# Kernel tuning notes

Measured on AMD Instinct MI355X. Metric: run time of the kernel, lower is better.

## Reference

```python
import jax, jax.numpy as jnp
import numpy as np

B, S, H = 2, 2048, 2048
NQ, NKV, DH = 16, 8, 128
EPS = 1e-6
ROPE_BASE = 10000.0


def setup_inputs() -> dict:
    key = jax.random.key(0)
    ks = jax.random.split(key, 6)
    hidden_states = jax.random.normal(ks[0], (B, S, H), dtype=jnp.float32)
    # real RoPE tables
    inv_freq = 1.0 / (ROPE_BASE ** (jnp.arange(0, DH, 2, dtype=jnp.float32) / DH))
    pos = jnp.arange(S, dtype=jnp.float32)
    freqs = pos[:, None] * inv_freq[None, :]              # [S, DH/2]
    emb = jnp.concatenate([freqs, freqs], axis=-1)        # [S, DH]
    cos = jnp.broadcast_to(jnp.cos(emb)[None], (B, S, DH))
    sin = jnp.broadcast_to(jnp.sin(emb)[None], (B, S, DH))
    # additive causal mask [1,1,S,S]
    causal = jnp.tril(jnp.ones((S, S), dtype=bool))
    attention_mask = jnp.where(causal, 0.0, jnp.finfo(jnp.float32).min)[None, None]
    q_w = jax.random.normal(ks[1], (H, H), dtype=jnp.float32) * 0.02
    k_w = jax.random.normal(ks[2], (NKV * DH, H), dtype=jnp.float32) * 0.02
    v_w = jax.random.normal(ks[3], (NKV * DH, H), dtype=jnp.float32) * 0.02
    o_w = jax.random.normal(ks[4], (H, H), dtype=jnp.float32) * 0.02
    return {"hidden_states": hidden_states, "cos": cos, "sin": sin,
            "attention_mask": attention_mask,
            "q_w": q_w, "k_w": k_w, "v_w": v_w, "o_w": o_w}


def _rotate_half(x):
    x1, x2 = jnp.split(x, 2, axis=-1)
    return jnp.concatenate([-x2, x1], axis=-1)


def _l2norm(x, eps=EPS):
    # weightless RMS norm over head_dim (Llama4TextL2Norm)
    return x * jax.lax.rsqrt(jnp.mean(x * x, axis=-1, keepdims=True) + eps)


def reference(hidden_states, cos, sin, attention_mask, q_w, k_w, v_w, o_w):
    b, s, _ = hidden_states.shape
    # projections (no bias) -> [B, n_heads, S, DH]
    q = jnp.einsum('bsh,dh->bsd', hidden_states, q_w).reshape(b, s, NQ, DH).transpose(0, 2, 1, 3)
    k = jnp.einsum('bsh,dh->bsd', hidden_states, k_w).reshape(b, s, NKV, DH).transpose(0, 2, 1, 3)
    v = jnp.einsum('bsh,dh->bsd', hidden_states, v_w).reshape(b, s, NKV, DH).transpose(0, 2, 1, 3)
    # NanoChat negates sin before standard HF rotary
    sin_e = (-sin)[:, None, :, :]   # [B,1,S,DH]
    cos_e = cos[:, None, :, :]
    q = q * cos_e + _rotate_half(q) * sin_e
    k = k * cos_e + _rotate_half(k) * sin_e
    # weightless QK RMS norm
    q = _l2norm(q)
    k = _l2norm(k)
    # GQA: repeat kv heads
    groups = NQ // NKV
    k = jnp.repeat(k, groups, axis=1)
    v = jnp.repeat(v, groups, axis=1)
    scaling = DH ** -0.5
    scores = jnp.einsum('bhqd,bhkd->bhqk', q, k) * scaling + attention_mask
    probs = jax.nn.softmax(scores, axis=-1)
    attn = jnp.einsum('bhqk,bhkd->bhqd', probs, v)           # [B,H,S,DH]
    attn = attn.transpose(0, 2, 1, 3).reshape(b, s, NQ * DH)
    out = jnp.einsum('bsd,hd->bsh', attn, o_w)
    return out
```

## Files before the change

kernel.cpp:

```cpp
#include <hip/hip_runtime.h>

typedef unsigned short ushort_t;
typedef __bf16 bf16x8 __attribute__((ext_vector_type(8)));
typedef float f32x4 __attribute__((ext_vector_type(4)));
typedef unsigned int u32x4 __attribute__((ext_vector_type(4)));
typedef unsigned short us4 __attribute__((ext_vector_type(4)));
typedef unsigned short us8 __attribute__((ext_vector_type(8)));

#define DEVINL __device__ __forceinline__

DEVINL ushort_t f2bf(float f) {
    unsigned u = __float_as_uint(f);
    u += 0x7FFF + ((u >> 16) & 1);
    return (ushort_t)(u >> 16);
}
DEVINL float bf2f(ushort_t h) { return __uint_as_float(((unsigned)h) << 16); }

DEVINL void gload_lds16(const void* g, void* l) {
    __builtin_amdgcn_global_load_lds(
        (const __attribute__((address_space(1))) void*)g,
        (__attribute__((address_space(3))) void*)l, 16, 0, 0);
}

DEVINL bf16x8 ld_frag(const ushort_t* p) {
    us8 v = *(const us8*)p;
    return __builtin_bit_cast(bf16x8, v);
}

#define BAR()     asm volatile("s_barrier" ::: "memory")
#define LGKM0()   asm volatile("s_waitcnt lgkmcnt(0)" ::: "memory")
#define VMCNT(n)  asm volatile("s_waitcnt vmcnt(" #n ")" ::: "memory")

#define BARRIER_KEEP4()  asm volatile("s_waitcnt vmcnt(4)\n\ts_barrier" ::: "memory")
#define BARRIER_KEEP8()  asm volatile("s_waitcnt vmcnt(8)\n\ts_barrier" ::: "memory")
#define BARRIER_KEEP0()  asm volatile("s_waitcnt vmcnt(0)\n\ts_barrier" ::: "memory")

__global__ __launch_bounds__(256) void convert_all(const f32x4* __restrict__ h,
                                                   const f32x4* __restrict__ qw,
                                                   const f32x4* __restrict__ kw,
                                                   const f32x4* __restrict__ vw,
                                                   const f32x4* __restrict__ ow,
                                                   us4* __restrict__ hb,
                                                   us4* __restrict__ wqkv,
                                                   us4* __restrict__ owb) {
    const int N0 = 2097152;
    const int N1 = 1048576;
    const int N2 = 524288;
    const int N3 = 524288;
    int i = blockIdx.x * 256 + threadIdx.x;
    const f32x4* src; us4* dst;
    if (i < N0)                               { src = h  + i;                 dst = hb + i; }
    else if ((i -= N0) < N1)                  { src = qw + i;                 dst = wqkv + i; }
    else if ((i -= N1) < N2)                  { src = kw + i;                 dst = wqkv + 1048576 + i; }
    else if ((i -= N2) < N3)                  { src = vw + i;                 dst = wqkv + 1572864 + i; }
    else                                      { i -= N3; src = ow + i;       dst = owb + i; }
    f32x4 f = *src;
    us4 o;
    o[0] = f2bf(f[0]); o[1] = f2bf(f[1]); o[2] = f2bf(f[2]); o[3] = f2bf(f[3]);
    *dst = o;
}

template <typename OutT>
__global__ __launch_bounds__(512, 2) void gemm256(const ushort_t* __restrict__ A,
                                                  const ushort_t* __restrict__ W,
                                                  OutT* __restrict__ C,
                                                  int N, int K) {
    __shared__ ushort_t As[2][256 * 64];
    __shared__ ushort_t Bs[2][256 * 64];
    const int t = threadIdx.x;
    const int lane = t & 63;
    const int quad = lane >> 4, l16 = lane & 15;
    const int wm = t >> 8, wn = (t >> 6) & 3;

    int bid = blockIdx.x;
    int xcd = bid & 7, j = bid >> 3;
    int tm, tn;
    if (N == 4096) { tm = (xcd >> 1) * 4 + (j >> 3); tn = (xcd & 1) * 8 + (j & 7); }
    else           { tm = xcd * 2 + (j >> 3);        tn = j & 7; }
    const int bm = tm * 256, bn = tn * 256;

    const int srow0 = t >> 3;
    const int sg0 = ((t & 7) ^ (srow0 & 7)) * 8;
    const int srow1 = srow0 + 64;
    const int sg1 = ((t & 7) ^ (srow1 & 7)) * 8;

    auto stageA = [&](int buf, int half, int k0) {
        gload_lds16(A + (size_t)(bm + half * 128 + srow0) * K + k0 + sg0,
                    &As[buf][half * 8192 + t * 8]);
        gload_lds16(A + (size_t)(bm + half * 128 + srow1) * K + k0 + sg1,
                    &As[buf][half * 8192 + 4096 + t * 8]);
    };
    auto stageB = [&](int buf, int half, int k0) {
        gload_lds16(W + (size_t)(bn + half * 128 + srow0) * K + k0 + sg0,
                    &Bs[buf][half * 8192 + t * 8]);
        gload_lds16(W + (size_t)(bn + half * 128 + srow1) * K + k0 + sg1,
                    &Bs[buf][half * 8192 + 4096 + t * 8]);
    };

    const int xsw = l16 & 7;
    const int arow = (wm * 128 + l16) * 64;
    const int brow = (wn * 64 + l16) * 64;
    const int ac0 = ((0 + quad) ^ xsw) * 8;
    const int ac1 = ((4 + quad) ^ xsw) * 8;

    auto ldA = [&](int buf, int mf, int kk) {
        return ld_frag(&As[buf][arow + mf * 1024 + (kk ? ac1 : ac0)]);
    };
    auto ldB = [&](int buf, int nf, int kk) {
        return ld_frag(&Bs[buf][brow + nf * 1024 + (kk ? ac1 : ac0)]);
    };

    f32x4 acc[8][4];
#pragma unroll
    for (int i = 0; i < 8; i++)
#pragma unroll
        for (int jj = 0; jj < 4; jj++) acc[i][jj] = f32x4{0.f, 0.f, 0.f, 0.f};

    const int NIT = K >> 6;
    stageA(0, 0, 0); stageA(0, 1, 0); stageB(0, 0, 0); stageB(0, 1, 0);
    VMCNT(4);
    stageB(1, 0, 64); stageB(1, 1, 64); stageA(1, 0, 64);
    VMCNT(6);
    BAR();

    bf16x8 a[4][2], b[4][2];
    for (int tt = 0; tt < NIT; ++tt) {
        const int buf = tt & 1;
        const int k2 = (tt + 2) << 6;

#pragma unroll
        for (int mt = 0; mt < 4; mt++) { a[mt][0] = ldA(buf, mt, 0); a[mt][1] = ldA(buf, mt, 1); }
#pragma unroll
        for (int nt = 0; nt < 4; nt++) { b[nt][0] = ldB(buf, nt, 0); b[nt][1] = ldB(buf, nt, 1); }
        if (tt + 1 < NIT) stageA(buf ^ 1, 1, (tt + 1) << 6);
        BAR(); LGKM0();
        __builtin_amdgcn_s_setprio(1);
#pragma unroll
        for (int mt = 0; mt < 4; mt++)
#pragma unroll
            for (int nt = 0; nt < 2; nt++)
#pragma unroll
                for (int kk = 0; kk < 2; kk++)
                    acc[mt][nt] = __builtin_amdgcn_mfma_f32_16x16x32_bf16(a[mt][kk], b[nt][kk], acc[mt][nt], 0, 0, 0);
        __builtin_amdgcn_s_setprio(0);
        LGKM0();
        BAR();

        if (tt + 2 < NIT) stageB(buf, 0, k2);
        BAR();
        __builtin_amdgcn_s_setprio(1);
#pragma unroll
        for (int mt = 0; mt < 4; mt++)
#pragma unroll
            for (int nt = 0; nt < 2; nt++)
#pragma unroll
                for (int kk = 0; kk < 2; kk++)
                    acc[mt][2 + nt] = __builtin_amdgcn_mfma_f32_16x16x32_bf16(a[mt][kk], b[2 + nt][kk], acc[mt][2 + nt], 0, 0, 0);
        __builtin_amdgcn_s_setprio(0);
        BAR();

#pragma unroll
        for (int mt = 0; mt < 4; mt++) { a[mt][0] = ldA(buf, 4 + mt, 0); a[mt][1] = ldA(buf, 4 + mt, 1); }
        if (tt + 2 < NIT) stageB(buf, 1, k2);
        BAR(); LGKM0();
        __builtin_amdgcn_s_setprio(1);
#pragma unroll
        for (int mt = 0; mt < 4; mt++)
#pragma unroll
            for (int nt = 0; nt < 2; nt++)
#pragma unroll
                for (int kk = 0; kk < 2; kk++)
                    acc[4 + mt][nt] = __builtin_amdgcn_mfma_f32_16x16x32_bf16(a[mt][kk], b[nt][kk], acc[4 + mt][nt], 0, 0, 0);
        __builtin_amdgcn_s_setprio(0);
        BAR();

        if (tt + 2 < NIT)      { stageA(buf, 0, k2); VMCNT(6); }
        else if (tt + 1 < NIT) { VMCNT(0); }
        BAR();
        __builtin_amdgcn_s_setprio(1);
#pragma unroll
        for (int mt = 0; mt < 4; mt++)
#pragma unroll
            for (int nt = 0; nt < 2; nt++)
#pragma unroll
                for (int kk = 0; kk < 2; kk++)
                    acc[4 + mt][2 + nt] = __builtin_amdgcn_mfma_f32_16x16x32_bf16(a[mt][kk], b[2 + nt][kk], acc[4 + mt][2 + nt], 0, 0, 0);
        __builtin_amdgcn_s_setprio(0);
        BAR();
    }

#pragma unroll
    for (int mf = 0; mf < 8; mf++)
#pragma unroll
        for (int nf = 0; nf < 4; nf++) {
            const int row = bm + wm * 128 + mf * 16 + quad * 4;
            const int col = bn + wn * 64 + nf * 16 + l16;
#pragma unroll
            for (int rr = 0; rr < 4; rr++) {
                float v = acc[mf][nf][rr];
                if constexpr (sizeof(OutT) == 2)
                    C[(size_t)(row + rr) * N + col] = (OutT)f2bf(v);
                else
                    C[(size_t)(row + rr) * N + col] = v;
            }
        }
}

__global__ __launch_bounds__(256) void rope_norm(const ushort_t* __restrict__ qkv,
                                                 const float* __restrict__ cosb,
                                                 const float* __restrict__ sinb,
                                                 ushort_t* __restrict__ q,
                                                 ushort_t* __restrict__ k) {
    int row = blockIdx.x;
    int b = row >> 11, s = row & 2047;
    int w = threadIdx.x >> 6, lane = threadIdx.x & 63;
    int hh = blockIdx.y * 4 + w;
    const ushort_t* src = qkv + (size_t)row * 4096 + hh * 128;
    float x1 = bf2f(src[lane]);
    float x2 = bf2f(src[lane + 64]);
    float c = cosb[(size_t)row * 128 + lane];
    float sn = sinb[(size_t)row * 128 + lane];
    float y1 = x1 * c + x2 * sn;
    float y2 = x2 * c - x1 * sn;
    float ss = y1 * y1 + y2 * y2;
#pragma unroll
    for (int off = 1; off < 64; off <<= 1) ss += __shfl_xor(ss, off);
    float rinv = rsqrtf(ss * (1.0f / 128.0f) + 1e-6f);
    y1 *= rinv; y2 *= rinv;
    ushort_t* dst;
    if (hh < 16) dst = q + (((size_t)(b * 16 + hh)) * 2048 + s) * 128;
    else         dst = k + (((size_t)(b * 8 + hh - 16)) * 2048 + s) * 128;
    dst[lane] = f2bf(y1);
    dst[lane + 64] = f2bf(y2);
}

__global__ __launch_bounds__(256) void v_transpose(const ushort_t* __restrict__ qkv,
                                                   ushort_t* __restrict__ vt) {
    __shared__ ushort_t tile[64 * 72];
    int t = threadIdx.x;
    int s0 = blockIdx.x * 64, d0 = blockIdx.y * 64, bh = blockIdx.z;
    int b = bh >> 3, kvh = bh & 7;
    {
        int sl = t >> 2, c = t & 3;
        const ushort_t* src = qkv + (size_t)(b * 2048 + s0 + sl) * 4096 + 3072 + kvh * 128 + d0 + c * 16;
        u32x4 v0 = *(const u32x4*)src;
        u32x4 v1 = *(const u32x4*)(src + 8);
        *(u32x4*)&tile[sl * 72 + c * 16] = v0;
        *(u32x4*)&tile[sl * 72 + c * 16 + 8] = v1;
    }
    __syncthreads();
    {
        int dl = t >> 2, c = t & 3;
        alignas(16) ushort_t tmp[16];
#pragma unroll
        for (int i = 0; i < 16; i++) tmp[i] = tile[(c * 16 + i) * 72 + dl];
        ushort_t* dst = vt + (size_t)(bh * 128 + d0 + dl) * 2048 + s0 + c * 16;
        *(u32x4*)dst = *(const u32x4*)&tmp[0];
        *(u32x4*)(dst + 8) = *(const u32x4*)&tmp[8];
    }
}

__global__ __launch_bounds__(256) void flash_attn(const ushort_t* __restrict__ q,
                                                  const ushort_t* __restrict__ k,
                                                  const ushort_t* __restrict__ vt,
                                                  ushort_t* __restrict__ attn) {
    __shared__ ushort_t Ks[3][4 * 64 * 32];
    __shared__ ushort_t Vts[3][2 * 128 * 32];
    __shared__ ushort_t Ps[4 * 32 * 72];
    const int t = threadIdx.x;
    const int w = t >> 6, lane = t & 63;
    const int quad = lane >> 4, l16 = lane & 15;
    const int sw = (l16 >> 1) & 3;
    const int lid = blockIdx.x;
    const int xcd = lid & 7, jj = lid >> 3;
    const int g = xcd * 2 + (jj >> 4);
    const int p = jj & 15;
    const int b = g >> 3, kvh = g & 7;
    const int h0 = kvh * 2;
    const size_t kbase = ((size_t)(b * 8 + kvh)) * 2048 * 128;
    const size_t vbase = ((size_t)(b * 8 + kvh)) * 128 * 2048;

    const float C1 = 0.12751744f;
    const float C2 = 1.45f;

    auto stage = [&](int j0, int buf) {
#pragma unroll
        for (int i = 0; i < 4; i++) {
            int u = i * 256 + t;
            int qd = u >> 8, rr = (u >> 2) & 63;
            int c4 = ((u & 3) ^ ((rr >> 1) & 3)) * 8;
            gload_lds16(k + kbase + (size_t)(j0 + rr) * 128 + qd * 32 + c4,
                        (char*)Ks[buf] + u * 16);
        }
#pragma unroll
        for (int i = 0; i < 4; i++) {
            int u = i * 256 + t;
            int ks = u >> 9, dd = (u >> 2) & 127;
            int c4 = ((u & 3) ^ ((dd >> 1) & 3)) * 8;
            gload_lds16(vt + vbase + (size_t)dd * 2048 + j0 + ks * 32 + c4,
                        (char*)Vts[buf] + u * 16);
        }
    };

    const int qtile0 = 31 - p;
    const int S_total = qtile0 + 1 + p + 1;
    auto j0_of = [&](int s) { return (s <= qtile0 ? s : s - qtile0 - 1) * 64; };

    stage(j0_of(0), 0);
    stage(j0_of(1), 1);
    int sidx = 0, cb = 0, pb = 2;

    for (int pass = 0; pass < 2; ++pass) {
        const int qi = pass ? p : qtile0;
        const int q0 = qi * 64;

        bf16x8 qf[2][4];
#pragma unroll
        for (int h = 0; h < 2; h++) {
            const size_t qbase = ((size_t)(b * 16 + h0 + h) * 2048 + q0 + w * 16 + l16) * 128;
#pragma unroll
            for (int qd = 0; qd < 4; qd++) {
                us8 v = *(const us8*)(q + qbase + qd * 32 + quad * 8);
                qf[h][qd] = __builtin_bit_cast(bf16x8, v);
            }
        }

        f32x4 o[2][8];
#pragma unroll
        for (int h = 0; h < 2; h++)
#pragma unroll
            for (int i = 0; i < 8; i++) o[h][i] = f32x4{0.f, 0.f, 0.f, 0.f};
        float lsum[2][4];
#pragma unroll
        for (int h = 0; h < 2; h++)
#pragma unroll
            for (int r = 0; r < 4; r++) lsum[h][r] = 0.f;

        for (int jt = 0; jt <= qi; ++jt) {
            const int j0 = jt * 64;
            const bool diag = (jt == qi);
            if (sidx + 1 < S_total) BARRIER_KEEP8();
            else                    BARRIER_KEEP0();
            if (sidx + 2 < S_total) stage(j0_of(sidx + 2), pb);
            const ushort_t* Kb = Ks[cb];
            const ushort_t* Vb = Vts[cb];
            cb = cb == 2 ? 0 : cb + 1;
            pb = pb == 2 ? 0 : pb + 1;
            sidx++;

            f32x4 sc[2][4];
#pragma unroll
            for (int h = 0; h < 2; h++)
#pragma unroll
                for (int c = 0; c < 4; c++) sc[h][c] = f32x4{0.f, 0.f, 0.f, 0.f};
#pragma unroll
            for (int c = 0; c < 4; c++)
#pragma unroll
                for (int qd = 0; qd < 4; qd++) {
                    bf16x8 kf = ld_frag(&Kb[qd * 2048 + (c * 16 + l16) * 32 + (quad ^ sw) * 8]);
                    sc[0][c] = __builtin_amdgcn_mfma_f32_16x16x32_bf16(qf[0][qd], kf, sc[0][c], 0, 0, 0);
                    sc[1][c] = __builtin_amdgcn_mfma_f32_16x16x32_bf16(qf[1][qd], kf, sc[1][c], 0, 0, 0);
                }

#pragma unroll
            for (int c = 0; c < 4; c++)
#pragma unroll
                for (int r = 0; r < 4; r++) {
                    float p0 = __builtin_amdgcn_exp2f(sc[0][c][r] * C1 - C2);
                    float p1 = __builtin_amdgcn_exp2f(sc[1][c][r] * C1 - C2);
                    if (diag) {
                        int kg = j0 + c * 16 + l16;
                        int qg = q0 + w * 16 + quad * 4 + r;
                        if (kg > qg) { p0 = 0.f; p1 = 0.f; }
                    }
                    lsum[0][r] += p0;
                    lsum[1][r] += p1;
                    Ps[w * 2304 + (quad * 4 + r) * 72 + c * 16 + l16] = f2bf(p0);
                    Ps[w * 2304 + (16 + quad * 4 + r) * 72 + c * 16 + l16] = f2bf(p1);
                }

#pragma unroll
            for (int ks = 0; ks < 2; ks++) {
                bf16x8 pf0 = ld_frag(&Ps[w * 2304 + l16 * 72 + ks * 32 + quad * 8]);
                bf16x8 pf1 = ld_frag(&Ps[w * 2304 + (16 + l16) * 72 + ks * 32 + quad * 8]);
#pragma unroll
                for (int od = 0; od < 8; od++) {
                    bf16x8 vf = ld_frag(&Vb[ks * 4096 + (od * 16 + l16) * 32 + (quad ^ sw) * 8]);
                    o[0][od] = __builtin_amdgcn_mfma_f32_16x16x32_bf16(pf0, vf, o[0][od], 0, 0, 0);
                    o[1][od] = __builtin_amdgcn_mfma_f32_16x16x32_bf16(pf1, vf, o[1][od], 0, 0, 0);
                }
            }
        }

        float rl[2][4];
#pragma unroll
        for (int h = 0; h < 2; h++)
#pragma unroll
            for (int r = 0; r < 4; r++) {
                float s = lsum[h][r];
#pragma unroll
                for (int off = 1; off < 16; off <<= 1) s += __shfl_xor(s, off);
                rl[h][r] = 1.0f / s;
            }
#pragma unroll
        for (int h = 0; h < 2; h++) {
            const size_t obase = ((size_t)(b * 2048 + q0 + w * 16 + quad * 4)) * 2048 + (h0 + h) * 128;
#pragma unroll
            for (int od = 0; od < 8; od++)
#pragma unroll
                for (int r = 0; r < 4; r++)
                    attn[obase + (size_t)r * 2048 + od * 16 + l16] = f2bf(o[h][od][r] * rl[h][r]);
        }
    }
}

extern "C" void kernel_launch(void* const* d_in, const int* in_sizes, int n_in,
                              void* d_out, int out_size, void* d_ws, size_t ws_size,
                              hipStream_t stream) {
    (void)in_sizes; (void)n_in; (void)out_size; (void)ws_size;
    const float* hidden = (const float*)d_in[0];
    const float* cosb   = (const float*)d_in[1];
    const float* sinb   = (const float*)d_in[2];
    const float* q_w    = (const float*)d_in[4];
    const float* k_w    = (const float*)d_in[5];
    const float* v_w    = (const float*)d_in[6];
    const float* o_w    = (const float*)d_in[7];

    char* ws = (char*)d_ws;
    ushort_t* hb   = (ushort_t*)(ws);
    ushort_t* wqkv = (ushort_t*)(ws + (16ull << 20));
    ushort_t* owb  = (ushort_t*)(ws + (32ull << 20));
    ushort_t* qkv  = (ushort_t*)(ws + (40ull << 20));
    ushort_t* attn = qkv;
    ushort_t* qb   = (ushort_t*)(ws + (72ull << 20));
    ushort_t* kb   = (ushort_t*)(ws + (88ull << 20));
    ushort_t* vt   = (ushort_t*)(ws + (96ull << 20));

    convert_all<<<20480, 256, 0, stream>>>((const f32x4*)hidden, (const f32x4*)q_w,
                                           (const f32x4*)k_w, (const f32x4*)v_w,
                                           (const f32x4*)o_w,
                                           (us4*)hb, (us4*)wqkv, (us4*)owb);

    gemm256<ushort_t><<<256, 512, 0, stream>>>(hb, wqkv, qkv, 4096, 2048);
    rope_norm<<<dim3(4096, 6), 256, 0, stream>>>(qkv, cosb, sinb, qb, kb);
    v_transpose<<<dim3(32, 2, 16), 256, 0, stream>>>(qkv, vt);
    flash_attn<<<256, 256, 0, stream>>>(qb, kb, vt, attn);
    gemm256<float><<<128, 512, 0, stream>>>(attn, owb, (float*)d_out, 2048, 2048);
}
```

Baseline: 352.9 us.

## Split flash attention work across 8 waves with shared P tile and row-sum reduction

Doubles the flash attention block to 512 threads. Each pair of waves now splits the key columns for QK^T and the output head-dim for PV, so per-wave accumulators and MFMA work are halved. To support this, the P tile is shared across the wave pair, with an extra barrier each iteration, and the softmax row sums are combined through a small LDS buffer. It also raises wave priority around the MFMA sections. The aim is more waves per CU to hide latency, at the cost of one additional block-wide barrier per key tile and a redundant Q fragment load in both waves of a pair.

```diff
diff --git a/kernel.cpp b/kernel.cpp
--- a/kernel.cpp
+++ b/kernel.cpp
@@ -32,7 +32,6 @@
 #define VMCNT(n)  asm volatile("s_waitcnt vmcnt(" #n ")" ::: "memory")
 
 #define BARRIER_KEEP4()  asm volatile("s_waitcnt vmcnt(4)\n\ts_barrier" ::: "memory")
-#define BARRIER_KEEP8()  asm volatile("s_waitcnt vmcnt(8)\n\ts_barrier" ::: "memory")
 #define BARRIER_KEEP0()  asm volatile("s_waitcnt vmcnt(0)\n\ts_barrier" ::: "memory")
 
 __global__ __launch_bounds__(256) void convert_all(const f32x4* __restrict__ h,
@@ -260,15 +259,17 @@
     }
 }
 
-__global__ __launch_bounds__(256) void flash_attn(const ushort_t* __restrict__ q,
+__global__ __launch_bounds__(512) void flash_attn(const ushort_t* __restrict__ q,
                                                   const ushort_t* __restrict__ k,
                                                   const ushort_t* __restrict__ vt,
                                                   ushort_t* __restrict__ attn) {
     __shared__ ushort_t Ks[3][4 * 64 * 32];
     __shared__ ushort_t Vts[3][2 * 128 * 32];
-    __shared__ ushort_t Ps[4 * 32 * 72];
+    __shared__ ushort_t Ps[2 * 64 * 72];
+    __shared__ float    Lred[2][4][2][16];
     const int t = threadIdx.x;
     const int w = t >> 6, lane = t & 63;
+    const int w4 = w & 3, wh = w >> 2;
     const int quad = lane >> 4, l16 = lane & 15;
     const int sw = (l16 >> 1) & 3;
     const int lid = blockIdx.x;
@@ -285,16 +286,16 @@
 
     auto stage = [&](int j0, int buf) {
 #pragma unroll
-        for (int i = 0; i < 4; i++) {
-            int u = i * 256 + t;
+        for (int i = 0; i < 2; i++) {
+            int u = i * 512 + t;
             int qd = u >> 8, rr = (u >> 2) & 63;
             int c4 = ((u & 3) ^ ((rr >> 1) & 3)) * 8;
             gload_lds16(k + kbase + (size_t)(j0 + rr) * 128 + qd * 32 + c4,
                         (char*)Ks[buf] + u * 16);
         }
 #pragma unroll
-        for (int i = 0; i < 4; i++) {
-            int u = i * 256 + t;
+        for (int i = 0; i < 2; i++) {
+            int u = i * 512 + t;
             int ks = u >> 9, dd = (u >> 2) & 127;
             int c4 = ((u & 3) ^ ((dd >> 1) & 3)) * 8;
             gload_lds16(vt + vbase + (size_t)dd * 2048 + j0 + ks * 32 + c4,
@@ -317,7 +318,7 @@
         bf16x8 qf[2][4];
 #pragma unroll
         for (int h = 0; h < 2; h++) {
-            const size_t qbase = ((size_t)(b * 16 + h0 + h) * 2048 + q0 + w * 16 + l16) * 128;
+            const size_t qbase = ((size_t)(b * 16 + h0 + h) * 2048 + q0 + w4 * 16 + l16) * 128;
 #pragma unroll
             for (int qd = 0; qd < 4; qd++) {
                 us8 v = *(const us8*)(q + qbase + qd * 32 + quad * 8);
@@ -325,11 +326,11 @@
             }
         }
 
-        f32x4 o[2][8];
+        f32x4 o[2][4];
 #pragma unroll
         for (int h = 0; h < 2; h++)
 #pragma unroll
-            for (int i = 0; i < 8; i++) o[h][i] = f32x4{0.f, 0.f, 0.f, 0.f};
+            for (int i = 0; i < 4; i++) o[h][i] = f32x4{0.f, 0.f, 0.f, 0.f};
         float lsum[2][4];
 #pragma unroll
         for (int h = 0; h < 2; h++)
@@ -339,7 +340,7 @@
         for (int jt = 0; jt <= qi; ++jt) {
             const int j0 = jt * 64;
             const bool diag = (jt == qi);
-            if (sidx + 1 < S_total) BARRIER_KEEP8();
+            if (sidx + 1 < S_total) BARRIER_KEEP4();
             else                    BARRIER_KEEP0();
             if (sidx + 2 < S_total) stage(j0_of(sidx + 2), pb);
             const ushort_t* Kb = Ks[cb];
@@ -348,48 +349,56 @@
             pb = pb == 2 ? 0 : pb + 1;
             sidx++;
 
-            f32x4 sc[2][4];
+            f32x4 sc[2][2];
 #pragma unroll
             for (int h = 0; h < 2; h++)
 #pragma unroll
-                for (int c = 0; c < 4; c++) sc[h][c] = f32x4{0.f, 0.f, 0.f, 0.f};
-#pragma unroll
-            for (int c = 0; c < 4; c++)
+                for (int c = 0; c < 2; c++) sc[h][c] = f32x4{0.f, 0.f, 0.f, 0.f};
+            __builtin_amdgcn_s_setprio(1);
+#pragma unroll
+            for (int c = 0; c < 2; c++)
 #pragma unroll
                 for (int qd = 0; qd < 4; qd++) {
-                    bf16x8 kf = ld_frag(&Kb[qd * 2048 + (c * 16 + l16) * 32 + (quad ^ sw) * 8]);
+                    bf16x8 kf = ld_frag(&Kb[qd * 2048 + ((wh * 2 + c) * 16 + l16) * 32 + (quad ^ sw) * 8]);
                     sc[0][c] = __builtin_amdgcn_mfma_f32_16x16x32_bf16(qf[0][qd], kf, sc[0][c], 0, 0, 0);
                     sc[1][c] = __builtin_amdgcn_mfma_f32_16x16x32_bf16(qf[1][qd], kf, sc[1][c], 0, 0, 0);
                 }
-
-#pragma unroll
-            for (int c = 0; c < 4; c++)
+            __builtin_amdgcn_s_setprio(0);
+
+#pragma unroll
+            for (int c = 0; c < 2; c++)
 #pragma unroll
                 for (int r = 0; r < 4; r++) {
                     float p0 = __builtin_amdgcn_exp2f(sc[0][c][r] * C1 - C2);
                     float p1 = __builtin_amdgcn_exp2f(sc[1][c][r] * C1 - C2);
                     if (diag) {
-                        int kg = j0 + c * 16 + l16;
-                        int qg = q0 + w * 16 + quad * 4 + r;
+                        int kg = j0 + wh * 32 + c * 16 + l16;
+                        int qg = q0 + w4 * 16 + quad * 4 + r;
                         if (kg > qg) { p0 = 0.f; p1 = 0.f; }
                     }
                     lsum[0][r] += p0;
                     lsum[1][r] += p1;
-                    Ps[w * 2304 + (quad * 4 + r) * 72 + c * 16 + l16] = f2bf(p0);
-                    Ps[w * 2304 + (16 + quad * 4 + r) * 72 + c * 16 + l16] = f2bf(p1);
+                    int prow = w4 * 16 + quad * 4 + r;
+                    int pcol = wh * 32 + c * 16 + l16;
+                    Ps[prow * 72 + pcol] = f2bf(p0);
+                    Ps[4608 + prow * 72 + pcol] = f2bf(p1);
                 }
-
+            LGKM0();
+            BAR();
+
+            __builtin_amdgcn_s_setprio(1);
 #pragma unroll
             for (int ks = 0; ks < 2; ks++) {
-                bf16x8 pf0 = ld_frag(&Ps[w * 2304 + l16 * 72 + ks * 32 + quad * 8]);
-                bf16x8 pf1 = ld_frag(&Ps[w * 2304 + (16 + l16) * 72 + ks * 32 + quad * 8]);
-#pragma unroll
-                for (int od = 0; od < 8; od++) {
-                    bf16x8 vf = ld_frag(&Vb[ks * 4096 + (od * 16 + l16) * 32 + (quad ^ sw) * 8]);
+                bf16x8 pf0 = ld_frag(&Ps[(w4 * 16 + l16) * 72 + ks * 32 + quad * 8]);
+                bf16x8 pf1 = ld_frag(&Ps[4608 + (w4 * 16 + l16) * 72 + ks * 32 + quad * 8]);
+#pragma unroll
+                for (int od = 0; od < 4; od++) {
+                    bf16x8 vf = ld_frag(&Vb[ks * 4096 + (wh * 64 + od * 16 + l16) * 32 + (quad ^ sw) * 8]);
                     o[0][od] = __builtin_amdgcn_mfma_f32_16x16x32_bf16(pf0, vf, o[0][od], 0, 0, 0);
                     o[1][od] = __builtin_amdgcn_mfma_f32_16x16x32_bf16(pf1, vf, o[1][od], 0, 0, 0);
                 }
             }
+            __builtin_amdgcn_s_setprio(0);
         }
 
         float rl[2][4];
@@ -400,13 +409,22 @@
                 float s = lsum[h][r];
 #pragma unroll
                 for (int off = 1; off < 16; off <<= 1) s += __shfl_xor(s, off);
-                rl[h][r] = 1.0f / s;
+                if (l16 == 0) Lred[wh][w4][h][quad * 4 + r] = s;
             }
+        LGKM0();
+        BAR();
+#pragma unroll
+        for (int h = 0; h < 2; h++)
+#pragma unroll
+            for (int r = 0; r < 4; r++)
+                rl[h][r] = 1.0f / (Lred[0][w4][h][quad * 4 + r] + Lred[1][w4][h][quad * 4 + r]);
+
 #pragma unroll
         for (int h = 0; h < 2; h++) {
-            const size_t obase = ((size_t)(b * 2048 + q0 + w * 16 + quad * 4)) * 2048 + (h0 + h) * 128;
-#pragma unroll
-            for (int od = 0; od < 8; od++)
+            const size_t obase = ((size_t)(b * 2048 + q0 + w4 * 16 + quad * 4)) * 2048
+                                 + (h0 + h) * 128 + wh * 64;
+#pragma unroll
+            for (int od = 0; od < 4; od++)
 #pragma unroll
                 for (int r = 0; r < 4; r++)
                     attn[obase + (size_t)r * 2048 + od * 16 + l16] = f2bf(o[h][od][r] * rl[h][r]);
@@ -444,6 +462,6 @@
     gemm256<ushort_t><<<256, 512, 0, stream>>>(hb, wqkv, qkv, 4096, 2048);
     rope_norm<<<dim3(4096, 6), 256, 0, stream>>>(qkv, cosb, sinb, qb, kb);
     v_transpose<<<dim3(32, 2, 16), 256, 0, stream>>>(qkv, vt);
-    flash_attn<<<256, 256, 0, stream>>>(qb, kb, vt, attn);
+    flash_attn<<<256, 512, 0, stream>>>(qb, kb, vt, attn);
     gemm256<float><<<128, 512, 0, stream>>>(attn, owb, (float*)d_out, 2048, 2048);
 }
```

Measured after the change: 349.8 us. No clear change (-0.9%).
